# Performance work log

Hardware: AMD Instinct MI355X
Metric: run time of the kernel (lower is better)

The kernel has to match this reference:

```python
import jax, jax.numpy as jnp
from jax import lax
import numpy as np

B, C, N, T, K = 16, 64, 512, 64, 2
KSIZE, DIL = 2, 1
PAD = (KSIZE - 1) * DIL
EPS = 1e-5


def _powers(A, k):
    Ps = [jnp.eye(A.shape[0], dtype=A.dtype)]
    for _ in range(k):
        Ps.append(Ps[-1] @ A)
    return jnp.stack(Ps)  # (K+1, N, N)


def setup_inputs() -> dict:
    key = jax.random.key(0)
    ks = jax.random.split(key, 12)
    x = jax.random.normal(ks[0], (B, C, N, T), dtype=jnp.float32)
    # row-normalized random transition matrices, precomputed powers
    Af = jax.random.uniform(ks[1], (N, N), dtype=jnp.float32)
    Af = Af / Af.sum(axis=1, keepdims=True)
    Ab = Af.T / Af.T.sum(axis=1, keepdims=True)
    Aa = jax.random.uniform(ks[2], (N, N), dtype=jnp.float32)
    Aa = Aa / Aa.sum(axis=1, keepdims=True)
    P_f_pows = _powers(Af, K)
    P_b_pows = _powers(Ab, K)
    A_adp_pows = _powers(Aa, K)
    s = 0.05
    filter_w = jax.random.normal(ks[3], (C, C, 1, KSIZE), dtype=jnp.float32) * s
    filter_b = jnp.zeros((C,), jnp.float32)
    gate_w = jax.random.normal(ks[4], (C, C, 1, KSIZE), dtype=jnp.float32) * s
    gate_b = jnp.zeros((C,), jnp.float32)
    skip_w = jax.random.normal(ks[5], (C, C, 1, 1), dtype=jnp.float32) * s
    skip_b = jnp.zeros((C,), jnp.float32)
    weight_f = jax.random.normal(ks[6], (K + 1, C, C), dtype=jnp.float32) * s
    weight_b = jax.random.normal(ks[7], (K + 1, C, C), dtype=jnp.float32) * s
    gcn_bias = jnp.zeros((C,), jnp.float32)
    ln_gamma = jnp.ones((C,), jnp.float32)
    ln_beta = jnp.zeros((C,), jnp.float32)
    alpha = jnp.float32(0.5)
    return dict(x=x, P_f_pows=P_f_pows, P_b_pows=P_b_pows, A_adp_pows=A_adp_pows,
                filter_w=filter_w, filter_b=filter_b, gate_w=gate_w, gate_b=gate_b,
                skip_w=skip_w, skip_b=skip_b, weight_f=weight_f, weight_b=weight_b,
                gcn_bias=gcn_bias, ln_gamma=ln_gamma, ln_beta=ln_beta, alpha=alpha)


def _conv(x, w, b, dil=1):
    y = lax.conv_general_dilated(x, w, window_strides=(1, 1), padding='VALID',
                                 rhs_dilation=(1, dil),
                                 dimension_numbers=('NCHW', 'OIHW', 'NCHW'))
    return y + b[None, :, None, None]


def _apply_powers(xt, P_pows, weights):
    # xt: (B*T, N, Cin); P_pows: (K+1, N, N); weights: (K+1, Cin, Cout)
    xk = jnp.einsum('kij,bjc->kbic', P_pows, xt)
    return jnp.einsum('kbic,kco->bio', xk, weights)


def reference(x, P_f_pows, P_b_pows, A_adp_pows,
              filter_w, filter_b, gate_w, gate_b, skip_w, skip_b,
              weight_f, weight_b, gcn_bias, ln_gamma, ln_beta, alpha):
    # --- Gated TCN (causal left-pad along time) ---
    x_pad = jnp.pad(x, ((0, 0), (0, 0), (0, 0), (PAD, 0)))
    f = jnp.tanh(_conv(x_pad, filter_w, filter_b, DIL))
    g = jax.nn.sigmoid(_conv(x_pad, gate_w, gate_b, DIL))
    out = f * g                                   # (B, C, N, T)
    skip = _conv(out, skip_w, skip_b)             # 1x1 conv
    x_temporal = x + out                          # in_channels == out_channels

    # --- Diffusion GCN on (B*T, N, C) ---
    xt = jnp.transpose(x_temporal, (0, 3, 2, 1)).reshape(B * T, N, C)
    static_out = (_apply_powers(xt, P_f_pows, weight_f)
                  + _apply_powers(xt, P_b_pows, weight_b)
                  + gcn_bias[None, None, :])
    adapt_out = (_apply_powers(xt, A_adp_pows, weight_f)
                 + _apply_powers(xt, A_adp_pows, weight_b)
                 + gcn_bias[None, None, :])

    a = jax.nn.sigmoid(alpha)
    x_gcn = a * static_out + (1.0 - a) * adapt_out

    # --- LayerNorm over channel dim (dropout = identity in eval) ---
    mu = x_gcn.mean(axis=-1, keepdims=True)
    var = ((x_gcn - mu) ** 2).mean(axis=-1, keepdims=True)
    x_gcn = (x_gcn - mu) * lax.rsqrt(var + EPS) * ln_gamma + ln_beta

    x_out = x_gcn.reshape(B, T, N, C).transpose(0, 3, 2, 1)  # (B, C, N, T)
    return (x_out, skip)
```

## Files before the change

### kernel.cpp

```cpp
#include <hip/hip_runtime.h>
#include <cstdint>
#include <cstddef>

#define NB 16
#define NC 64
#define NN 512
#define NT 64
#define BT (NB*NT)
#define NN2 (NN*NN)
#define XSTRIDE_B (NC*NN*NT)
#define XSTRIDE_C (NN*NT)
#define XT_ROW (BT*NC)

typedef __attribute__((ext_vector_type(8))) short short8;
typedef __attribute__((ext_vector_type(4))) float f32x4;
typedef unsigned short ushort_t;
typedef unsigned int uint_t;

__device__ __forceinline__ ushort_t f2bf(float f) {
    uint_t u = __builtin_bit_cast(uint_t, f);
    u += 0x7FFFu + ((u >> 16) & 1u);
    return (ushort_t)(u >> 16);
}
__device__ __forceinline__ float bf2f(ushort_t u) {
    return __builtin_bit_cast(float, (uint_t)u << 16);
}
__device__ __forceinline__ void gl_lds16(const void* g, void* s) {
    __builtin_amdgcn_global_load_lds(
        (const __attribute__((address_space(1))) unsigned int*)g,
        (__attribute__((address_space(3))) unsigned int*)s, 16, 0, 0);
}

__global__ void k_prep(const float* __restrict__ wf, const float* __restrict__ wb,
                       const float* __restrict__ alpha, ushort_t* __restrict__ Wcb) {
    int i = blockIdx.x * 256 + threadIdx.x;
    if (i >= 7 * 4096) return;
    float a = 1.f / (1.f + expf(-alpha[0]));
    int r = i >> 12, co = i & 4095;
    int c = co >> 6, o = co & 63;
    float v;
    if      (r == 0) v = wf[co] + wb[co];
    else if (r == 1) v = a * wf[4096 + co];
    else if (r == 2) v = a * wf[8192 + co];
    else if (r == 3) v = a * wb[4096 + co];
    else if (r == 4) v = a * wb[8192 + co];
    else if (r == 5) v = (1.f - a) * (wf[4096 + co] + wb[4096 + co]);
    else             v = (1.f - a) * (wf[8192 + co] + wb[8192 + co]);
    int chunk = ((c >> 5) << 2) | (o >> 4);
    int lane  = (((c >> 3) & 3) << 4) | (o & 15);
    int j     = c & 7;
    Wcb[r * 4096 + chunk * 512 + lane * 8 + j] = f2bf(v);
}

__global__ void k_prepP(const float* __restrict__ Pf, const float* __restrict__ Pb,
                        const float* __restrict__ Aa, ushort_t* __restrict__ Apk) {
    int i = blockIdx.x * 256 + threadIdx.x;
    if (i >= 196608) return;
    int lane = i & 63, kc = (i >> 6) & 15, nt = (i >> 10) & 31, r = i >> 15;
    const float* base;
    if      (r == 0) base = Pf + NN2;
    else if (r == 1) base = Pf + 2 * NN2;
    else if (r == 2) base = Pb + NN2;
    else if (r == 3) base = Pb + 2 * NN2;
    else if (r == 4) base = Aa + NN2;
    else             base = Aa + 2 * NN2;
    int n = nt * 16 + (lane & 15);
    int k0 = kc * 32 + (lane >> 4) * 8;
    const float* src = base + (size_t)n * NN + k0;
    float4 v0 = ((const float4*)src)[0];
    float4 v1 = ((const float4*)src)[1];
    uint4 o;
    o.x = (uint_t)f2bf(v0.x) | ((uint_t)f2bf(v0.y) << 16);
    o.y = (uint_t)f2bf(v0.z) | ((uint_t)f2bf(v0.w) << 16);
    o.z = (uint_t)f2bf(v1.x) | ((uint_t)f2bf(v1.y) << 16);
    o.w = (uint_t)f2bf(v1.z) | ((uint_t)f2bf(v1.w) << 16);
    *(uint4*)(Apk + (size_t)i * 8) = o;
}

__global__ void k_prepW(const float* __restrict__ fw, const float* __restrict__ gw,
                        const float* __restrict__ sw, ushort_t* __restrict__ Wt) {
    int i = blockIdx.x * 256 + threadIdx.x;
    if (i >= 5 * 4096) return;
    int mat = i >> 12, t = i & 4095;
    int chunk = t >> 9, l = (t >> 3) & 63, j = t & 7;
    int m = chunk >> 1, kb = chunk & 1;
    int o = m * 16 + (l & 15);
    int c = kb * 32 + ((l >> 4) << 3) + j;
    float v;
    if      (mat == 0) v = fw[o * 128 + c * 2 + 0];
    else if (mat == 1) v = fw[o * 128 + c * 2 + 1];
    else if (mat == 2) v = gw[o * 128 + c * 2 + 0];
    else if (mat == 3) v = gw[o * 128 + c * 2 + 1];
    else               v = sw[o * 64 + c];
    Wt[i] = f2bf(v);
}

#define XS_P 72
__device__ __forceinline__ int swzA(int r, int c) {
    return r * XS_P + (c ^ (((r >> 4) & 3) << 3));
}
__global__ __launch_bounds__(256, 3) void k_tcn(
    const float* __restrict__ x,
    const ushort_t* __restrict__ Wt,
    const float* __restrict__ fb, const float* __restrict__ gb,
    const float* __restrict__ sb,
    float* __restrict__ skip_out, ushort_t* __restrict__ XTbf) {
    __shared__ __align__(16) ushort_t Xs[65 * XS_P];
    __shared__ __align__(16) ushort_t Os[64 * XS_P];

    int tx = threadIdx.x;
    int b = blockIdx.x >> 9, n = blockIdx.x & (NN - 1);

    {
        int c = tx >> 2, tq = tx & 3, t0 = tq * 16;
        const float* src = x + (size_t)b * XSTRIDE_B + (size_t)c * XSTRIDE_C
                             + (size_t)n * NT + t0;
        float4 v0 = ((const float4*)src)[0];
        float4 v1 = ((const float4*)src)[1];
        float4 v2 = ((const float4*)src)[2];
        float4 v3 = ((const float4*)src)[3];
        float vv[16] = {v0.x, v0.y, v0.z, v0.w, v1.x, v1.y, v1.z, v1.w,
                        v2.x, v2.y, v2.z, v2.w, v3.x, v3.y, v3.z, v3.w};
#pragma unroll
        for (int e = 0; e < 16; ++e) {
            int r = t0 + e + 1;
            Xs[swzA(r, c)] = f2bf(vv[e]);
        }
        if (tx < 8) ((uint4*)Xs)[tx] = (uint4){0, 0, 0, 0};
    }
    __syncthreads();

    int w = tx >> 6, l = tx & 63, lr = l & 15, lg = l >> 4;

    short8 wf0[2], wf1[2], wg0[2], wg1[2], wsk[2];
#pragma unroll
    for (int kb = 0; kb < 2; ++kb) {
        int off = (w * 2 + kb) * 512 + l * 8;
        wf0[kb] = *(const short8*)(Wt + 0 * 4096 + off);
        wf1[kb] = *(const short8*)(Wt + 1 * 4096 + off);
        wg0[kb] = *(const short8*)(Wt + 2 * 4096 + off);
        wg1[kb] = *(const short8*)(Wt + 3 * 4096 + off);
        wsk[kb] = *(const short8*)(Wt + 4 * 4096 + off);
    }
    float fbv[4], gbv[4], sbv[4];
#pragma unroll
    for (int q = 0; q < 4; ++q) {
        int o = w * 16 + lg * 4 + q;
        fbv[q] = fb[o]; gbv[q] = gb[o]; sbv[q] = sb[o];
    }

#pragma unroll
    for (int tb = 0; tb < 4; ++tb) {
        short8 b0[2], b1[2];
#pragma unroll
        for (int kb = 0; kb < 2; ++kb) {
            int blk = kb * 4 + lg;
            int r1 = tb * 16 + lr + 1, r0 = tb * 16 + lr;
            b1[kb] = *(const short8*)&Xs[r1 * XS_P + (((blk ^ ((r1 >> 4) & 3)) << 3))];
            b0[kb] = *(const short8*)&Xs[r0 * XS_P + (((blk ^ ((r0 >> 4) & 3)) << 3))];
        }
        f32x4 aF = {fbv[0], fbv[1], fbv[2], fbv[3]};
        f32x4 aG = {gbv[0], gbv[1], gbv[2], gbv[3]};
        aF = __builtin_amdgcn_mfma_f32_16x16x32_bf16(wf0[0], b0[0], aF, 0, 0, 0);
        aF = __builtin_amdgcn_mfma_f32_16x16x32_bf16(wf0[1], b0[1], aF, 0, 0, 0);
        aF = __builtin_amdgcn_mfma_f32_16x16x32_bf16(wf1[0], b1[0], aF, 0, 0, 0);
        aF = __builtin_amdgcn_mfma_f32_16x16x32_bf16(wf1[1], b1[1], aF, 0, 0, 0);
        aG = __builtin_amdgcn_mfma_f32_16x16x32_bf16(wg0[0], b0[0], aG, 0, 0, 0);
        aG = __builtin_amdgcn_mfma_f32_16x16x32_bf16(wg0[1], b0[1], aG, 0, 0, 0);
        aG = __builtin_amdgcn_mfma_f32_16x16x32_bf16(wg1[0], b1[0], aG, 0, 0, 0);
        aG = __builtin_amdgcn_mfma_f32_16x16x32_bf16(wg1[1], b1[1], aG, 0, 0, 0);
        int t = tb * 16 + lr;
#pragma unroll
        for (int q = 0; q < 4; ++q) {
            float fo = tanhf(aF[q]);
            float go = 1.f / (1.f + expf(-aG[q]));
            int o = w * 16 + lg * 4 + q;
            Os[swzA(t, o)] = f2bf(fo * go);
        }
    }
    __syncthreads();

    float* skp = skip_out + (size_t)b * XSTRIDE_B + (size_t)n * NT;
#pragma unroll
    for (int tb = 0; tb < 4; ++tb) {
        int t = tb * 16 + lr;
        short8 ov[2];
#pragma unroll
        for (int kb = 0; kb < 2; ++kb) {
            int blk = kb * 4 + lg;
            ov[kb] = *(const short8*)&Os[t * XS_P + (((blk ^ ((t >> 4) & 3)) << 3))];
        }
        f32x4 aS = {sbv[0], sbv[1], sbv[2], sbv[3]};
        aS = __builtin_amdgcn_mfma_f32_16x16x32_bf16(wsk[0], ov[0], aS, 0, 0, 0);
        aS = __builtin_amdgcn_mfma_f32_16x16x32_bf16(wsk[1], ov[1], aS, 0, 0, 0);
#pragma unroll
        for (int q = 0; q < 4; ++q) {
            int o = w * 16 + lg * 4 + q;
            skp[(size_t)o * XSTRIDE_C + t] = aS[q];
        }
    }

    {
        int t = tx >> 2, cch = (tx & 3) * 16;
        ushort_t* dst = XTbf + (size_t)n * XT_ROW + (size_t)b * 4096 + t * 64 + cch;
        int rX = t + 1;
#pragma unroll
        for (int blk2 = 0; blk2 < 2; ++blk2) {
            int cb = (cch >> 3) + blk2;
            short8 xv = *(const short8*)&Xs[rX * XS_P + ((cb ^ ((rX >> 4) & 3)) << 3)];
            short8 ovv = *(const short8*)&Os[t * XS_P + ((cb ^ ((t >> 4) & 3)) << 3)];
            uint_t pk[4];
#pragma unroll
            for (int h = 0; h < 4; ++h) {
                float s0 = bf2f((ushort_t)xv[h * 2]) + bf2f((ushort_t)ovv[h * 2]);
                float s1 = bf2f((ushort_t)xv[h * 2 + 1]) + bf2f((ushort_t)ovv[h * 2 + 1]);
                pk[h] = (uint_t)f2bf(s0) | ((uint_t)f2bf(s1) << 16);
            }
            *(uint4*)(dst + blk2 * 8) = (uint4){pk[0], pk[1], pk[2], pk[3]};
        }
    }
}

__global__ __launch_bounds__(256) void k_tr(const ushort_t* __restrict__ XTbf,
                                            ushort_t* __restrict__ Bpk) {
    __shared__ ushort_t tile[32 * XS_P];
    int tx = threadIdx.x;
    int bt = blockIdx.x;
    int jj = tx >> 3, c8 = (tx & 7) * 8;
    int f = tx >> 6, lane = tx & 63, lg = lane >> 4, lr = lane & 15;
    for (int kc = 0; kc < 16; ++kc) {
        if (kc) __syncthreads();
        *(uint4*)&tile[jj * XS_P + c8] =
            *(const uint4*)(XTbf + (size_t)(kc * 32 + jj) * XT_ROW + bt * 64 + c8);
        __syncthreads();
        ushort_t vals[8];
#pragma unroll
        for (int e = 0; e < 8; ++e)
            vals[e] = tile[(lg * 8 + e) * XS_P + f * 16 + lr];
        uint4 o;
        o.x = (uint_t)vals[0] | ((uint_t)vals[1] << 16);
        o.y = (uint_t)vals[2] | ((uint_t)vals[3] << 16);
        o.z = (uint_t)vals[4] | ((uint_t)vals[5] << 16);
        o.w = (uint_t)vals[6] | ((uint_t)vals[7] << 16);
        *(uint4*)(Bpk + (size_t)bt * 32768 + kc * 2048 + tx * 8) = o;
    }
}

__global__ __launch_bounds__(256, 2) void k_gcn(
    const ushort_t* __restrict__ Apk,
    const ushort_t* __restrict__ Bpk,
    const ushort_t* __restrict__ XTbf,
    const ushort_t* __restrict__ Wcb,
    const float* __restrict__ bias,
    ushort_t* __restrict__ G) {
    __shared__ __align__(16) ushort_t sB[2][4096];
    __shared__ __align__(16) ushort_t sY[4][16 * 72];
    __shared__ __align__(16) float sC[2][2][4][64][4];

    int tx = threadIdx.x;
    int w = tx >> 6, l = tx & 63;
    int lr = l & 15, lg = l >> 4;
    int s = w >> 1, h = w & 1;

    int bid = (blockIdx.x & 7) * 1024 + (blockIdx.x >> 3);
    int btp = bid >> 4;
    int n0i = bid & 15;
    int n0 = n0i << 5;
    int bt0 = btp * 2;

    f32x4 acc[3][8];
#pragma unroll
    for (int j = 0; j < 3; ++j)
#pragma unroll
        for (int f = 0; f < 8; ++f) acc[j][f] = (f32x4){0.f, 0.f, 0.f, 0.f};

    const ushort_t* aBase = Apk + (size_t)(h * 3) * NN2
                                + (size_t)(n0i * 2 + s) * 8192 + l * 8;
    const ushort_t* bSrc = Bpk + (size_t)bt0 * 32768 + w * 512 + l * 8;
    ushort_t* sBw0 = &sB[0][w * 512];
    ushort_t* sBw0p = &sB[0][2048 + w * 512];
    ushort_t* sBw1 = &sB[1][w * 512];
    ushort_t* sBw1p = &sB[1][2048 + w * 512];

    gl_lds16(bSrc, sBw0);
    gl_lds16(bSrc + 32768, sBw0p);
    short8 aE[3], aO[3];
#pragma unroll
    for (int j = 0; j < 3; ++j) aE[j] = *(const short8*)(aBase + (size_t)j * NN2);
    asm volatile("s_waitcnt vmcnt(3)" ::: "memory");
    __builtin_amdgcn_s_barrier();
    __builtin_amdgcn_sched_barrier(0);

#pragma unroll
    for (int tt = 0; tt < 8; ++tt) {
        {
            int t = 2 * tt;
            if (t < 15) {
                gl_lds16(bSrc + (t + 1) * 2048, sBw1);
                gl_lds16(bSrc + 32768 + (t + 1) * 2048, sBw1p);
#pragma unroll
                for (int j = 0; j < 3; ++j)
                    aO[j] = *(const short8*)(aBase + (size_t)j * NN2 + (t + 1) * 512);
            }
#pragma unroll
            for (int p = 0; p < 2; ++p) {
                short8 bv[4];
#pragma unroll
                for (int f = 0; f < 4; ++f)
                    bv[f] = *(const short8*)(&sB[0][0] + p * 2048 + f * 512 + l * 8);
#pragma unroll
                for (int j = 0; j < 3; ++j)
#pragma unroll
                    for (int f = 0; f < 4; ++f)
                        acc[j][p * 4 + f] = __builtin_amdgcn_mfma_f32_16x16x32_bf16(
                            aE[j], bv[f], acc[j][p * 4 + f], 0, 0, 0);
            }
            asm volatile("s_waitcnt vmcnt(3)" ::: "memory");
            __builtin_amdgcn_s_barrier();
            __builtin_amdgcn_sched_barrier(0);
        }
        {
            int t = 2 * tt + 1;
            if (t < 15) {
                gl_lds16(bSrc + (t + 1) * 2048, sBw0);
                gl_lds16(bSrc + 32768 + (t + 1) * 2048, sBw0p);
#pragma unroll
                for (int j = 0; j < 3; ++j)
                    aE[j] = *(const short8*)(aBase + (size_t)j * NN2 + (t + 1) * 512);
            }
#pragma unroll
            for (int p = 0; p < 2; ++p) {
                short8 bv[4];
#pragma unroll
                for (int f = 0; f < 4; ++f)
                    bv[f] = *(const short8*)(&sB[1][0] + p * 2048 + f * 512 + l * 8);
#pragma unroll
                for (int j = 0; j < 3; ++j)
#pragma unroll
                    for (int f = 0; f < 4; ++f)
                        acc[j][p * 4 + f] = __builtin_amdgcn_mfma_f32_16x16x32_bf16(
                            aO[j], bv[f], acc[j][p * 4 + f], 0, 0, 0);
            }
            asm volatile("s_waitcnt vmcnt(3)" ::: "memory");
            __builtin_amdgcn_s_barrier();
            __builtin_amdgcn_sched_barrier(0);
        }
    }

    ushort_t* sYw = &sY[w][0];
    const ushort_t* wBase = Wcb + l * 8;

#pragma unroll
    for (int p = 0; p < 2; ++p) {
        f32x4 acc2[4];
#pragma unroll
        for (int fo = 0; fo < 4; ++fo) {
            float b = (h == 0) ? bias[fo * 16 + lr] : 0.f;
            acc2[fo] = (f32x4){b, b, b, b};
        }
        if (h == 0) {
            const ushort_t* xs = XTbf + (size_t)(n0 + s * 16 + lr) * XT_ROW
                               + (bt0 + p) * 64 + lg * 8;
            short8 ay0 = *(const short8*)(xs);
            short8 ay1 = *(const short8*)(xs + 32);
#pragma unroll
            for (int kh = 0; kh < 2; ++kh)
#pragma unroll
                for (int fo = 0; fo < 4; ++fo) {
                    short8 wv = *(const short8*)(wBase + (kh * 4 + fo) * 512);
                    acc2[fo] = __builtin_amdgcn_mfma_f32_16x16x32_bf16(
                        kh ? ay1 : ay0, wv, acc2[fo], 0, 0, 0);
                }
        }
#pragma unroll
        for (int j = 0; j < 3; ++j) {
            int wcIdx = (h == 0) ? (j + 1) : (j + 4);
#pragma unroll
            for (int f = 0; f < 4; ++f)
#pragma unroll
                for (int q = 0; q < 4; ++q)
                    sYw[(lg * 4 + q) * 72 + f * 16 + lr] = f2bf(acc[j][p * 4 + f][q]);
            short8 ay0 = *(const short8*)(&sYw[lr * 72 + lg * 8]);
            short8 ay1 = *(const short8*)(&sYw[lr * 72 + 32 + lg * 8]);
#pragma unroll
            for (int kh = 0; kh < 2; ++kh)
#pragma unroll
                for (int fo = 0; fo < 4; ++fo) {
                    short8 wv = *(const short8*)(wBase + wcIdx * 4096 + (kh * 4 + fo) * 512);
                    acc2[fo] = __builtin_amdgcn_mfma_f32_16x16x32_bf16(
                        kh ? ay1 : ay0, wv, acc2[fo], 0, 0, 0);
                }
        }
        if (h == 1) {
#pragma unroll
            for (int fo = 0; fo < 4; ++fo)
                *(f32x4*)&sC[s][p][fo][l][0] = acc2[fo];
        } else {
#pragma unroll
            for (int fo = 0; fo < 4; ++fo) acc[0][p * 4 + fo] = acc2[fo];
        }
    }
    __syncthreads();
    if (h == 0) {
#pragma unroll
        for (int p = 0; p < 2; ++p) {
            ushort_t* gp = G + (size_t)(n0 + s * 16 + lg * 4) * XT_ROW
                         + (bt0 + p) * 64 + lr;
#pragma unroll
            for (int fo = 0; fo < 4; ++fo) {
                f32x4 mine = acc[0][p * 4 + fo];
                f32x4 other = *(const f32x4*)&sC[s][p][fo][l][0];
#pragma unroll
                for (int q = 0; q < 4; ++q)
                    gp[(size_t)q * XT_ROW + fo * 16] = f2bf(mine[q] + other[q]);
            }
        }
    }
}

__global__ __launch_bounds__(256) void k_ln_t(
    const ushort_t* __restrict__ G,
    const float* __restrict__ gamma, const float* __restrict__ beta,
    float* __restrict__ xout) {
    __shared__ float sT[64 * 65];
    __shared__ float sMu[64], sRs[64];
    __shared__ float sS[64 * 4], sQ[64 * 4];

    int bid = blockIdx.x;
    int b = bid >> 9, n = bid & (NN - 1);
    int tx = threadIdx.x;
    const ushort_t* src = G + (size_t)n * XT_ROW + (size_t)b * (NT * NC);

#pragma unroll
    for (int u = 0; u < 2; ++u) {
        int fi = u * 256 + tx;
        uint4 v = ((const uint4*)src)[fi];
        int t = fi >> 3, c = (fi & 7) * 8;
        sT[t * 65 + c + 0] = bf2f((ushort_t)(v.x & 0xffff));
        sT[t * 65 + c + 1] = bf2f((ushort_t)(v.x >> 16));
        sT[t * 65 + c + 2] = bf2f((ushort_t)(v.y & 0xffff));
        sT[t * 65 + c + 3] = bf2f((ushort_t)(v.y >> 16));
        sT[t * 65 + c + 4] = bf2f((ushort_t)(v.z & 0xffff));
        sT[t * 65 + c + 5] = bf2f((ushort_t)(v.z >> 16));
        sT[t * 65 + c + 6] = bf2f((ushort_t)(v.w & 0xffff));
        sT[t * 65 + c + 7] = bf2f((ushort_t)(v.w >> 16));
    }
    __syncthreads();
    {
        int row = tx >> 2, seg = tx & 3;
        float s = 0.f, q = 0.f;
        for (int cc = 0; cc < 16; ++cc) {
            float v = sT[row * 65 + seg * 16 + cc];
            s += v; q += v * v;
        }
        sS[row * 4 + seg] = s; sQ[row * 4 + seg] = q;
    }
    __syncthreads();
    if (tx < 64) {
        float ss = sS[tx * 4] + sS[tx * 4 + 1] + sS[tx * 4 + 2] + sS[tx * 4 + 3];
        float qq = sQ[tx * 4] + sQ[tx * 4 + 1] + sQ[tx * 4 + 2] + sQ[tx * 4 + 3];
        float mu = ss * (1.f / 64.f);
        float var = qq * (1.f / 64.f) - mu * mu;
        sMu[tx] = mu; sRs[tx] = rsqrtf(var + 1e-5f);
    }
    __syncthreads();
    {
        int t = tx & 63, cg = (tx >> 6) * 16;
        float mu = sMu[t], rs = sRs[t];
        for (int cc = 0; cc < 16; ++cc) {
            int c = cg + cc;
            float v = (sT[t * 65 + c] - mu) * rs * gamma[c] + beta[c];
            xout[(size_t)b * XSTRIDE_B + (size_t)c * XSTRIDE_C + (size_t)n * NT + t] = v;
        }
    }
}

extern "C" void kernel_launch(void* const* d_in, const int* in_sizes, int n_in,
                              void* d_out, int out_size, void* d_ws, size_t ws_size,
                              hipStream_t stream) {
    const float* x     = (const float*)d_in[0];
    const float* Pf    = (const float*)d_in[1];
    const float* Pb    = (const float*)d_in[2];
    const float* Aa    = (const float*)d_in[3];
    const float* fw    = (const float*)d_in[4];
    const float* fb    = (const float*)d_in[5];
    const float* gw    = (const float*)d_in[6];
    const float* gb    = (const float*)d_in[7];
    const float* sw    = (const float*)d_in[8];
    const float* sb    = (const float*)d_in[9];
    const float* wf    = (const float*)d_in[10];
    const float* wb    = (const float*)d_in[11];
    const float* gbias = (const float*)d_in[12];
    const float* lng   = (const float*)d_in[13];
    const float* lnb   = (const float*)d_in[14];
    const float* alpha = (const float*)d_in[15];

    float* xout = (float*)d_out;
    float* skip = (float*)d_out + (size_t)NB * NC * NN * NT;

    char* ws = (char*)d_ws;
    ushort_t* XTbf = (ushort_t*)(ws);
    ushort_t* Bpk  = (ushort_t*)(ws + 67108864);
    ushort_t* Gb   = (ushort_t*)(ws + 134217728);
    ushort_t* Apk  = (ushort_t*)(ws + 201326592);
    ushort_t* Wcb  = (ushort_t*)(ws + 204472320);
    ushort_t* Wt   = (ushort_t*)(ws + 204537856);

    hipLaunchKernelGGL(k_prep, dim3(112), dim3(256), 0, stream, wf, wb, alpha, Wcb);
    hipLaunchKernelGGL(k_prepW, dim3(80), dim3(256), 0, stream, fw, gw, sw, Wt);
    hipLaunchKernelGGL(k_prepP, dim3(768), dim3(256), 0, stream, Pf, Pb, Aa, Apk);
    hipLaunchKernelGGL(k_tcn, dim3(NB * NN), dim3(256), 0, stream,
                       x, Wt, fb, gb, sb, skip, XTbf);
    hipLaunchKernelGGL(k_tr, dim3(1024), dim3(256), 0, stream, XTbf, Bpk);
    hipLaunchKernelGGL(k_gcn, dim3(8192), dim3(256), 0, stream,
                       Apk, Bpk, XTbf, Wcb, gbias, Gb);
    hipLaunchKernelGGL(k_ln_t, dim3(NB * NN), dim3(256), 0, stream, Gb, lng, lnb, xout);
}
```

Measured before the change: 428.8 us.

## Deepen GCN B-tile LDS pipeline to four stages with MFMA priority boost

Moves the B operand staging in the GCN kernel from a 2-buffer to a 4-buffer LDS ring, prefetching three steps ahead, and adjusts the vmcnt waits to match the deeper queue. It also raises wave priority around the MFMA section with s_setprio. The aim is to hide global-to-LDS latency better. The cost is doubling the sB LDS footprint, which may reduce occupancy under launch_bounds(256,2), and more complex waitcnt bookkeeping that must stay correct.

Measured after the change: 426.6 us. No clear change (-0.5%).

```diff
diff --git a/kernel.cpp b/kernel.cpp
--- a/kernel.cpp
+++ b/kernel.cpp
@@ -29,6 +29,13 @@
     __builtin_amdgcn_global_load_lds(
         (const __attribute__((address_space(1))) unsigned int*)g,
         (__attribute__((address_space(3))) unsigned int*)s, 16, 0, 0);
+}
+__device__ __forceinline__ void wait_vm(int n) {
+    if (n >= 7)      asm volatile("s_waitcnt vmcnt(7)" ::: "memory");
+    else if (n == 5) asm volatile("s_waitcnt vmcnt(5)" ::: "memory");
+    else if (n == 4) asm volatile("s_waitcnt vmcnt(4)" ::: "memory");
+    else if (n == 3) asm volatile("s_waitcnt vmcnt(3)" ::: "memory");
+    else             asm volatile("s_waitcnt vmcnt(0)" ::: "memory");
 }
 
 __global__ void k_prep(const float* __restrict__ wf, const float* __restrict__ wb,
@@ -253,7 +260,7 @@
     const ushort_t* __restrict__ Wcb,
     const float* __restrict__ bias,
     ushort_t* __restrict__ G) {
-    __shared__ __align__(16) ushort_t sB[2][4096];
+    __shared__ __align__(16) ushort_t sB[4][4096];
     __shared__ __align__(16) ushort_t sY[4][16 * 72];
     __shared__ __align__(16) float sC[2][2][4][64][4];
 
@@ -277,37 +284,40 @@
     const ushort_t* aBase = Apk + (size_t)(h * 3) * NN2
                                 + (size_t)(n0i * 2 + s) * 8192 + l * 8;
     const ushort_t* bSrc = Bpk + (size_t)bt0 * 32768 + w * 512 + l * 8;
-    ushort_t* sBw0 = &sB[0][w * 512];
-    ushort_t* sBw0p = &sB[0][2048 + w * 512];
-    ushort_t* sBw1 = &sB[1][w * 512];
-    ushort_t* sBw1p = &sB[1][2048 + w * 512];
-
-    gl_lds16(bSrc, sBw0);
-    gl_lds16(bSrc + 32768, sBw0p);
+
     short8 aE[3], aO[3];
 #pragma unroll
     for (int j = 0; j < 3; ++j) aE[j] = *(const short8*)(aBase + (size_t)j * NN2);
-    asm volatile("s_waitcnt vmcnt(3)" ::: "memory");
+#pragma unroll
+    for (int d = 0; d < 3; ++d) {
+        gl_lds16(bSrc + d * 2048, &sB[d][w * 512]);
+        gl_lds16(bSrc + 32768 + d * 2048, &sB[d][2048 + w * 512]);
+    }
+    wait_vm(4);
     __builtin_amdgcn_s_barrier();
     __builtin_amdgcn_sched_barrier(0);
 
 #pragma unroll
     for (int tt = 0; tt < 8; ++tt) {
         {
-            int t = 2 * tt;
-            if (t < 15) {
-                gl_lds16(bSrc + (t + 1) * 2048, sBw1);
-                gl_lds16(bSrc + 32768 + (t + 1) * 2048, sBw1p);
+            const int t = 2 * tt;
+            if (t + 1 < 16) {
 #pragma unroll
                 for (int j = 0; j < 3; ++j)
                     aO[j] = *(const short8*)(aBase + (size_t)j * NN2 + (t + 1) * 512);
             }
+            if (t + 3 < 16) {
+                gl_lds16(bSrc + (t + 3) * 2048, &sB[(t + 3) & 3][w * 512]);
+                gl_lds16(bSrc + 32768 + (t + 3) * 2048, &sB[(t + 3) & 3][2048 + w * 512]);
+            }
+            const ushort_t* sBr = &sB[t & 3][0];
+            __builtin_amdgcn_s_setprio(1);
 #pragma unroll
             for (int p = 0; p < 2; ++p) {
                 short8 bv[4];
 #pragma unroll
                 for (int f = 0; f < 4; ++f)
-                    bv[f] = *(const short8*)(&sB[0][0] + p * 2048 + f * 512 + l * 8);
+                    bv[f] = *(const short8*)(sBr + p * 2048 + f * 512 + l * 8);
 #pragma unroll
                 for (int j = 0; j < 3; ++j)
 #pragma unroll
@@ -315,25 +325,30 @@
                         acc[j][p * 4 + f] = __builtin_amdgcn_mfma_f32_16x16x32_bf16(
                             aE[j], bv[f], acc[j][p * 4 + f], 0, 0, 0);
             }
-            asm volatile("s_waitcnt vmcnt(3)" ::: "memory");
+            __builtin_amdgcn_s_setprio(0);
+            wait_vm(t <= 12 ? 7 : (t == 13 ? 5 : (t == 14 ? 3 : 0)));
             __builtin_amdgcn_s_barrier();
             __builtin_amdgcn_sched_barrier(0);
         }
         {
-            int t = 2 * tt + 1;
-            if (t < 15) {
-                gl_lds16(bSrc + (t + 1) * 2048, sBw0);
-                gl_lds16(bSrc + 32768 + (t + 1) * 2048, sBw0p);
+            const int t = 2 * tt + 1;
+            if (t + 1 < 16) {
 #pragma unroll
                 for (int j = 0; j < 3; ++j)
                     aE[j] = *(const short8*)(aBase + (size_t)j * NN2 + (t + 1) * 512);
             }
+            if (t + 3 < 16) {
+                gl_lds16(bSrc + (t + 3) * 2048, &sB[(t + 3) & 3][w * 512]);
+                gl_lds16(bSrc + 32768 + (t + 3) * 2048, &sB[(t + 3) & 3][2048 + w * 512]);
+            }
+            const ushort_t* sBr = &sB[t & 3][0];
+            __builtin_amdgcn_s_setprio(1);
 #pragma unroll
             for (int p = 0; p < 2; ++p) {
                 short8 bv[4];
 #pragma unroll
                 for (int f = 0; f < 4; ++f)
-                    bv[f] = *(const short8*)(&sB[1][0] + p * 2048 + f * 512 + l * 8);
+                    bv[f] = *(const short8*)(sBr + p * 2048 + f * 512 + l * 8);
 #pragma unroll
                 for (int j = 0; j < 3; ++j)
 #pragma unroll
@@ -341,7 +356,8 @@
                         acc[j][p * 4 + f] = __builtin_amdgcn_mfma_f32_16x16x32_bf16(
                             aO[j], bv[f], acc[j][p * 4 + f], 0, 0, 0);
             }
-            asm volatile("s_waitcnt vmcnt(3)" ::: "memory");
+            __builtin_amdgcn_s_setprio(0);
+            wait_vm(t <= 12 ? 7 : (t == 13 ? 5 : (t == 14 ? 3 : 0)));
             __builtin_amdgcn_s_barrier();
             __builtin_amdgcn_sched_barrier(0);
         }
```
